# Optimization experiments

Hardware: AMD Instinct MI355X
Metric: run time of the kernel (lower is better)

The kernel has to match this reference:

```python
import jax, jax.numpy as jnp
import numpy as np

B, N, C, M = 2, 16384, 256, 16  # M = win_w*win_h for stage 1
W = N // M

def setup_inputs() -> dict:
    key = jax.random.key(0)
    ks = jax.random.split(key, 8)
    s = 1.0 / np.sqrt(C)
    return {
        "input": jax.random.normal(ks[0], (B, N, C), jnp.float32),
        "embed_qk": jax.random.normal(ks[1], (B, W, M, M, 3), jnp.float32),
        "Wq": jax.random.normal(ks[2], (C, C), jnp.float32) * s,
        "bq": jax.random.normal(ks[3], (C,), jnp.float32) * 0.01,
        "Wk": jax.random.normal(ks[4], (C, C), jnp.float32) * s,
        "bk": jax.random.normal(ks[5], (C,), jnp.float32) * 0.01,
        "Wp": jax.random.normal(ks[6], (3, 1), jnp.float32) * 0.5,
        "bp": jax.random.normal(ks[7], (1,), jnp.float32) * 0.01,
    }

def reference(input, embed_qk, Wq, bq, Wk, bk, Wp, bp):
    WIN = 16  # stage==1 -> win_w*win_h = 4*4
    b, n, c = input.shape
    add = (-n) % WIN
    q = jax.nn.elu(input @ Wq + bq) + 1.0
    k = jax.nn.elu(input @ Wk + bk) + 1.0
    v = input
    pad = ((0, 0), (0, add), (0, 0))
    q_win = jnp.pad(q, pad).reshape(b, -1, WIN, c)
    k_win = jnp.pad(k, pad).reshape(b, -1, WIN, c)
    v_win = jnp.pad(v, pad).reshape(b, -1, WIN, c)
    # second ELU+1 feature map (as in the original)
    phi_q = jax.nn.elu(q_win) + 1.0
    phi_k = jax.nn.elu(k_win) + 1.0
    # KV sums over ALL windows w -> (b, m, c, d)
    KV = jnp.einsum('bwmc,bwmd->bmcd', phi_k, v_win)
    # (b, w, n, m, d) expanded intermediate
    att = jnp.einsum('bwnc,bmcd->bwnmd', phi_q, KV)
    p = (embed_qk @ Wp + bp)[..., 0]  # (b, w, m, m)
    att = att + p[..., None]
    out = att.reshape(b, -1, c)[:, :n, :]
    return out
```

## Files before the change

### kernel.cpp

```cpp
#include <hip/hip_runtime.h>

typedef __attribute__((ext_vector_type(8))) short s16x8;
typedef __attribute__((ext_vector_type(8))) ushort u16x8;
typedef __attribute__((ext_vector_type(4))) ushort u16x4;
typedef __attribute__((ext_vector_type(4))) float f32x4v;

namespace {

constexpr int kB = 2;
constexpr int kN = 16384;
constexpr int kC = 256;
constexpr int kQR = 1024;

__device__ __forceinline__ ushort f2bf(float f) {
  union { float f; uint u; } v; v.f = f;
  uint u = v.u + 0x7fffu + ((v.u >> 16) & 1u);
  return (ushort)(u >> 16);
}

__device__ __forceinline__ float phi_act(float x) {
  return x > 0.f ? x + 2.f : __expf(x) + 1.f;
}

__global__ __launch_bounds__(256) void wt_kernel(const float* __restrict__ Wq,
                                                 const float* __restrict__ Wk,
                                                 ushort* __restrict__ WqT,
                                                 ushort* __restrict__ WkT) {
  __shared__ float ts[64][65];
  const float* W = blockIdx.z ? Wk : Wq;
  ushort* WT = blockIdx.z ? WkT : WqT;
  const int bi = blockIdx.x, bj = blockIdx.y, t = threadIdx.x;
  for (int rep = 0; rep < 16; ++rep) {
    int e = rep * 256 + t, r = e >> 6, c = e & 63;
    ts[r][c] = W[(size_t)(bi * 64 + r) * kC + bj * 64 + c];
  }
  __syncthreads();
  for (int rep = 0; rep < 16; ++rep) {
    int e = rep * 256 + t, j = e >> 6, k = e & 63;
    WT[(size_t)(bj * 64 + j) * kC + bi * 64 + k] = f2bf(ts[k][j]);
  }
}

__global__ __launch_bounds__(256) void regroup_kernel(const float* __restrict__ X,
                                                      ushort* __restrict__ G) {
  __shared__ ushort ls[16 * 288];
  const int cb = blockIdx.x;
  const int wb = blockIdx.y;
  const int b = blockIdx.z;
  const int t = threadIdx.x;
  const float* src = X + ((size_t)b * kN + wb * 256) * kC + cb * 16;
  const int lr = t >> 2, cg = t & 3;
#pragma unroll
  for (int rep = 0; rep < 4; ++rep) {
    int row = rep * 64 + lr;
    float4 v = *reinterpret_cast<const float4*>(src + (size_t)row * kC + cg * 4);
    int w = row >> 4, m = row & 15;
    int base = w * 288 + m * 18 + cg * 4;
    uint p0 = (uint)f2bf(v.x) | ((uint)f2bf(v.y) << 16);
    uint p1 = (uint)f2bf(v.z) | ((uint)f2bf(v.w) << 16);
    *reinterpret_cast<uint*>(ls + base) = p0;
    *reinterpret_cast<uint*>(ls + base + 2) = p1;
  }
  __syncthreads();
  const int m = t >> 4, c_l = t & 15;
#pragma unroll
  for (int oct = 0; oct < 2; ++oct) {
    u16x8 v;
#pragma unroll
    for (int wl = 0; wl < 8; ++wl) v[wl] = ls[(oct * 8 + wl) * 288 + m * 18 + c_l];
    *reinterpret_cast<u16x8*>(
        G + (((size_t)(b * 16 + m) * 128 + wb * 2 + oct) * 256 + cb * 16 + c_l) * 8) = v;
  }
}

__global__ __launch_bounds__(256) void proj_kernel(
    const float* __restrict__ X, const ushort* __restrict__ WqT,
    const ushort* __restrict__ WkT, const float* __restrict__ bq,
    const float* __restrict__ bk, ushort* __restrict__ kg,
    ushort* __restrict__ qf) {
  __shared__ __align__(16) ushort smem[36864];

  const int t = threadIdx.x, lane = t & 63, wv = t >> 6;
  const int bx = blockIdx.x;
  const bool kmode = bx < 1024;
  int b, n0, jb;
  const ushort* WT;
  const float* bias;
  if (kmode) {
    b = bx >> 9; int rem = bx & 511; n0 = (rem >> 1) * 64; jb = bx & 1;
    WT = WkT; bias = bk;
  } else {
    int i = bx - 1024; b = i >> 5; int rem = i & 31; n0 = (rem >> 1) * 64; jb = i & 1;
    WT = WqT; bias = bq;
  }
  const int j0 = jb * 128;
  const float* Xb = X + ((size_t)b * kN + n0) * kC;

  for (int rep = 0; rep < 16; ++rep) {
    int idx = rep * 256 + t;
    int jj = idx >> 5, cc = idx & 31;
    u16x8 v = *reinterpret_cast<const u16x8*>(WT + (size_t)(j0 + jj) * kC + cc * 8);
    *reinterpret_cast<u16x8*>(smem + jj * 256 + ((cc ^ (jj & 31)) << 3)) = v;
  }

  const int aq = t & 7, ar = t >> 3;
  float4 fa0, fa1;
  auto aLoad = [&](int s) {
    fa0 = *reinterpret_cast<const float4*>(Xb + (size_t)ar * kC + s * 32 + aq * 4);
    fa1 = *reinterpret_cast<const float4*>(Xb + (size_t)(ar + 32) * kC + s * 32 + aq * 4);
  };
  auto aWrite = [&](int h) {
    ushort* A = smem + 32768 + h * 2048;
    u16x4 v0 = {f2bf(fa0.x), f2bf(fa0.y), f2bf(fa0.z), f2bf(fa0.w)};
    u16x4 v1 = {f2bf(fa1.x), f2bf(fa1.y), f2bf(fa1.z), f2bf(fa1.w)};
    *reinterpret_cast<u16x4*>(A + ar * 32 + (((aq >> 1) ^ ((ar >> 1) & 3)) << 3) +
                              (aq & 1) * 4) = v0;
    const int r1 = ar + 32;
    *reinterpret_cast<u16x4*>(A + r1 * 32 + (((aq >> 1) ^ ((r1 >> 1) & 3)) << 3) +
                              (aq & 1) * 4) = v1;
  };

  const int lo = lane & 15, hi = lane >> 4;
  const int wr0 = (wv >> 1) * 32, wc0 = (wv & 1) * 64;
  f32x4v acc[2][4] = {};
  auto mma = [&](int h, int s) {
    const ushort* A = smem + 32768 + h * 2048;
    s16x8 a[2], bf[4];
#pragma unroll
    for (int i = 0; i < 2; ++i) {
      int r = wr0 + i * 16 + lo;
      a[i] = *reinterpret_cast<const s16x8*>(A + r * 32 + ((hi ^ ((r >> 1) & 3)) << 3));
    }
#pragma unroll
    for (int fj = 0; fj < 4; ++fj) {
      int j = wc0 + fj * 16 + lo;
      bf[fj] = *reinterpret_cast<const s16x8*>(
          smem + j * 256 + (((s * 4 + hi) ^ (j & 31)) << 3));
    }
#pragma unroll
    for (int i = 0; i < 2; ++i)
#pragma unroll
      for (int fj = 0; fj < 4; ++fj)
        acc[i][fj] = __builtin_amdgcn_mfma_f32_16x16x32_bf16(a[i], bf[fj], acc[i][fj], 0, 0, 0);
  };

  aLoad(0);
  aWrite(0);
  __syncthreads();
  int cur = 0;
  for (int s = 0; s < 8; ++s) {
    if (s < 7) aLoad(s + 1);
    __builtin_amdgcn_sched_barrier(0);
    mma(cur, s);
    __builtin_amdgcn_sched_barrier(0);
    if (s < 7) aWrite(cur ^ 1);
    __syncthreads();
    cur ^= 1;
  }

  float bv[4];
#pragma unroll
  for (int fj = 0; fj < 4; ++fj) bv[fj] = bias[j0 + wc0 + fj * 16 + lo];

  if (kmode) {
    __syncthreads();
    ushort* ep = smem;
#pragma unroll
    for (int i = 0; i < 2; ++i)
#pragma unroll
      for (int fj = 0; fj < 4; ++fj)
#pragma unroll
        for (int r = 0; r < 4; ++r) {
          int row = wr0 + i * 16 + hi * 4 + r;
          int col = wc0 + fj * 16 + lo;
          ep[row * 128 + col] = f2bf(phi_act(acc[i][fj][r] + bv[fj]));
        }
    __syncthreads();
    const int m = t >> 4, cl = t & 15;
    const int wgrp = n0 >> 7, sub = (n0 >> 6) & 1;
#pragma unroll
    for (int rep = 0; rep < 8; ++rep) {
      int c = rep * 16 + cl;
      u16x4 v;
#pragma unroll
      for (int wl = 0; wl < 4; ++wl) v[wl] = ep[(wl * 16 + m) * 128 + c];
      *reinterpret_cast<u16x4*>(
          kg + (((size_t)(b * 16 + m) * 128 + wgrp) * 256 + j0 + c) * 8 + sub * 4) = v;
    }
  } else {
#pragma unroll
    for (int i = 0; i < 2; ++i)
#pragma unroll
      for (int fj = 0; fj < 4; ++fj)
#pragma unroll
        for (int r = 0; r < 4; ++r) {
          int row = n0 + wr0 + i * 16 + hi * 4 + r;
          int col = j0 + wc0 + fj * 16 + lo;
          qf[((size_t)b * kQR + row) * kC + col] = f2bf(phi_act(acc[i][fj][r] + bv[fj]));
        }
  }
}

__global__ __launch_bounds__(256) void kv_kernel(const ushort* __restrict__ kg,
                                                 const ushort* __restrict__ xg,
                                                 ushort* __restrict__ kvt) {
  __shared__ __align__(16) ushort smem[32768];
  const int t = threadIdx.x, lane = t & 63, wv = t >> 6;
  const int swz = (blockIdx.x & 7) * 64 + (blockIdx.x >> 3);
  const int bm = swz >> 4, cb = swz & 3, db = (swz >> 2) & 3;
  const int lc = t & 63, g = t >> 6;
  const ushort* Ab = kg + (size_t)bm * 262144 + (size_t)(cb * 64 + lc) * 8;
  const ushort* Bb = xg + (size_t)bm * 262144 + (size_t)(db * 64 + lc) * 8;

  u16x8 ra[4], rb[4];
  auto sLoad = [&](int s) {
#pragma unroll
    for (int q = 0; q < 4; ++q) {
      const size_t w8 = (size_t)(s * 16 + g + q * 4) * 2048;
      ra[q] = *reinterpret_cast<const u16x8*>(Ab + w8);
      rb[q] = *reinterpret_cast<const u16x8*>(Bb + w8);
    }
  };
  auto sWrite = [&](int h) {
    ushort* A = smem + h * 8192;
    ushort* B = smem + 16384 + h * 8192;
    const int fl = (lc & 15) ^ (lc >> 4);
#pragma unroll
    for (int q = 0; q < 4; ++q) {
      int o = g + q * 4;
      *reinterpret_cast<u16x8*>(A + lc * 128 + ((o ^ fl) << 3)) = ra[q];
      *reinterpret_cast<u16x8*>(B + lc * 128 + ((o ^ fl) << 3)) = rb[q];
    }
  };

  const int lo = lane & 15, hi = lane >> 4;
  const int wr0 = (wv >> 1) * 32, wc0 = (wv & 1) * 32;
  f32x4v acc[2][2] = {};
  auto mma = [&](int h) {
    const ushort* A = smem + h * 8192;
    const ushort* B = smem + 16384 + h * 8192;
#pragma unroll
    for (int kk = 0; kk < 4; ++kk) {
      s16x8 a0, a1, b0, b1;
      {
        int r = wr0 + lo;
        a0 = *reinterpret_cast<const s16x8*>(
            A + r * 128 + (((kk * 4 + hi) ^ ((r & 15) ^ (r >> 4))) << 3));
        int r2 = wr0 + 16 + lo;
        a1 = *reinterpret_cast<const s16x8*>(
            A + r2 * 128 + (((kk * 4 + hi) ^ ((r2 & 15) ^ (r2 >> 4))) << 3));
        int c = wc0 + lo;
        b0 = *reinterpret_cast<const s16x8*>(
            B + c * 128 + (((kk * 4 + hi) ^ ((c & 15) ^ (c >> 4))) << 3));
        int c2 = wc0 + 16 + lo;
        b1 = *reinterpret_cast<const s16x8*>(
            B + c2 * 128 + (((kk * 4 + hi) ^ ((c2 & 15) ^ (c2 >> 4))) << 3));
      }
      acc[0][0] = __builtin_amdgcn_mfma_f32_16x16x32_bf16(a0, b0, acc[0][0], 0, 0, 0);
      acc[0][1] = __builtin_amdgcn_mfma_f32_16x16x32_bf16(a0, b1, acc[0][1], 0, 0, 0);
      acc[1][0] = __builtin_amdgcn_mfma_f32_16x16x32_bf16(a1, b0, acc[1][0], 0, 0, 0);
      acc[1][1] = __builtin_amdgcn_mfma_f32_16x16x32_bf16(a1, b1, acc[1][1], 0, 0, 0);
    }
  };

  sLoad(0);
  sWrite(0);
  __syncthreads();
  int cur = 0;
  for (int s = 0; s < 8; ++s) {
    if (s < 7) sLoad(s + 1);
    __builtin_amdgcn_sched_barrier(0);
    mma(cur);
    __builtin_amdgcn_sched_barrier(0);
    if (s < 7) sWrite(cur ^ 1);
    __syncthreads();
    cur ^= 1;
  }
#pragma unroll
  for (int fi = 0; fi < 2; ++fi)
#pragma unroll
    for (int fj = 0; fj < 2; ++fj) {
      int d = db * 64 + wc0 + fj * 16 + lo;
      int c = cb * 64 + wr0 + fi * 16 + hi * 4;
      u16x4 v = {f2bf(acc[fi][fj][0]), f2bf(acc[fi][fj][1]),
                 f2bf(acc[fi][fj][2]), f2bf(acc[fi][fj][3])};
      *reinterpret_cast<u16x4*>(kvt + ((size_t)bm * 256 + d) * 256 + c) = v;
    }
}

__global__ __launch_bounds__(256) void out_kernel(
    const ushort* __restrict__ qf, const ushort* __restrict__ kvt,
    const float* __restrict__ EQK, const float* __restrict__ Wp,
    const float* __restrict__ bp, float* __restrict__ Out) {
  __shared__ __align__(16) ushort smem[16384];
  __shared__ float Ps[128];
  const int t = threadIdx.x, lane = t & 63, wv = t >> 6;
  const int swz = (blockIdx.x & 7) * 64 + (blockIdx.x >> 3);
  const int bm = swz >> 4, qb = swz & 7, db = (swz >> 3) & 1;
  const int b = bm >> 4, mm = bm & 15;
  if (t < 128) {
    int qr = qb * 128 + t;
    const float* e = EQK + (((size_t)(b * 1024 + (qr >> 4)) * 16 + (qr & 15)) * 16 + mm) * 3;
    Ps[t] = e[0] * Wp[0] + e[1] * Wp[1] + e[2] * Wp[2] + bp[0];
  }
  const int r2 = t >> 2, ch = t & 3;

  u16x8 ra0, ra1, rb0, rb1;
  auto stageLoad = [&](int ks) {
    int k0 = ks * 32;
    const ushort* Aq = qf + ((size_t)b * kQR + qb * 128) * kC;
    const ushort* Bk = kvt + ((size_t)bm * 256 + db * 128) * kC;
    ra0 = *reinterpret_cast<const u16x8*>(Aq + (size_t)r2 * kC + k0 + ch * 8);
    ra1 = *reinterpret_cast<const u16x8*>(Aq + (size_t)(r2 + 64) * kC + k0 + ch * 8);
    rb0 = *reinterpret_cast<const u16x8*>(Bk + (size_t)r2 * kC + k0 + ch * 8);
    rb1 = *reinterpret_cast<const u16x8*>(Bk + (size_t)(r2 + 64) * kC + k0 + ch * 8);
  };
  auto stageWrite = [&](int h) {
    ushort* A = smem + h * 4096;
    ushort* B = smem + 8192 + h * 4096;
    *reinterpret_cast<u16x8*>(A + r2 * 32 + ((ch ^ ((r2 >> 1) & 3)) << 3)) = ra0;
    *reinterpret_cast<u16x8*>(A + (r2 + 64) * 32 + ((ch ^ (((r2 + 64) >> 1) & 3)) << 3)) = ra1;
    *reinterpret_cast<u16x8*>(B + r2 * 32 + ((ch ^ ((r2 >> 1) & 3)) << 3)) = rb0;
    *reinterpret_cast<u16x8*>(B + (r2 + 64) * 32 + ((ch ^ (((r2 + 64) >> 1) & 3)) << 3)) = rb1;
  };

  f32x4v acc[4][4] = {};
  const int lo = lane & 15, hi = lane >> 4;
  const int wr0 = (wv >> 1) * 64, wc0 = (wv & 1) * 64;
  auto mma = [&](int h) {
    const ushort* A = smem + h * 4096;
    const ushort* B = smem + 8192 + h * 4096;
    s16x8 af[4], bf[4];
#pragma unroll
    for (int i = 0; i < 4; ++i) {
      int r = wr0 + i * 16 + lo;
      af[i] = *reinterpret_cast<const s16x8*>(A + r * 32 + ((hi ^ ((r >> 1) & 3)) << 3));
    }
#pragma unroll
    for (int j = 0; j < 4; ++j) {
      int c = wc0 + j * 16 + lo;
      bf[j] = *reinterpret_cast<const s16x8*>(B + c * 32 + ((hi ^ ((c >> 1) & 3)) << 3));
    }
#pragma unroll
    for (int i = 0; i < 4; ++i)
#pragma unroll
      for (int j = 0; j < 4; ++j)
        acc[i][j] = __builtin_amdgcn_mfma_f32_16x16x32_bf16(af[i], bf[j], acc[i][j], 0, 0, 0);
  };

  stageLoad(0);
  stageWrite(0);
  __syncthreads();
  int cur = 0;
  for (int ks = 0; ks < 8; ++ks) {
    if (ks < 7) stageLoad(ks + 1);
    __builtin_amdgcn_sched_barrier(0);
    mma(cur);
    __builtin_amdgcn_sched_barrier(0);
    if (ks < 7) stageWrite(cur ^ 1);
    __syncthreads();
    cur ^= 1;
  }
#pragma unroll
  for (int fi = 0; fi < 4; ++fi)
#pragma unroll
    for (int r4 = 0; r4 < 4; ++r4) {
      int rowl = wr0 + fi * 16 + hi * 4 + r4;
      int qr = qb * 128 + rowl;
      float p = Ps[rowl];
      size_t orow = ((size_t)b * kN + (size_t)qr * 16 + mm) * kC;
#pragma unroll
      for (int fj = 0; fj < 4; ++fj) {
        int d = db * 128 + wc0 + fj * 16 + lo;
        Out[orow + d] = acc[fi][fj][r4] + p;
      }
    }
}

}

extern "C" void kernel_launch(void* const* d_in, const int* in_sizes, int n_in,
                              void* d_out, int out_size, void* d_ws,
                              size_t ws_size, hipStream_t stream) {
  const float* input = (const float*)d_in[0];
  const float* eqk = (const float*)d_in[1];
  const float* Wq = (const float*)d_in[2];
  const float* bq = (const float*)d_in[3];
  const float* Wk = (const float*)d_in[4];
  const float* bk = (const float*)d_in[5];
  const float* Wp = (const float*)d_in[6];
  const float* bp = (const float*)d_in[7];
  float* out = (float*)d_out;

  ushort* ws = (ushort*)d_ws;
  ushort* WqT = ws;
  ushort* WkT = WqT + 65536;
  ushort* xg = WkT + 65536;
  ushort* kg = xg + 8388608;
  ushort* qf = kg + 8388608;
  ushort* kvt = qf + 524288;

  wt_kernel<<<dim3(4, 4, 2), 256, 0, stream>>>(Wq, Wk, WqT, WkT);
  regroup_kernel<<<dim3(16, 64, 2), 256, 0, stream>>>(input, xg);
  proj_kernel<<<dim3(1088), 256, 0, stream>>>(input, WqT, WkT, bq, bk, kg, qf);
  kv_kernel<<<dim3(512), 256, 0, stream>>>(kg, xg, kvt);
  out_kernel<<<dim3(512), 256, 0, stream>>>(qf, kvt, eqk, Wp, bp, out);
}
```

Before: 154.4 us.

## Use direct global-to-LDS loads in projection, KV, and output kernels

Replaces register-staged global loads followed by LDS writes with global_load_lds builtins in the projection weight staging, the KV reduction kernel, and the output GEMM. The KV kernel's LDS layout becomes k-major with no swizzle and keeps double buffering. The output kernel now loads the full K=256 tiles for A and B into 128 KB of LDS at once, replacing its 8-step pipelined loop, with the XOR swizzle moved to the global source address. This aims to cut VGPR pressure and instruction count for staging, but lower occupancy in out_kernel, lost overlap, and possible LDS bank conflicts in the unswizzled KV layout are risks.

```diff
diff --git a/kernel.cpp b/kernel.cpp
--- a/kernel.cpp
+++ b/kernel.cpp
@@ -20,6 +20,12 @@
 
 __device__ __forceinline__ float phi_act(float x) {
   return x > 0.f ? x + 2.f : __expf(x) + 1.f;
+}
+
+__device__ __forceinline__ void gl16(const ushort* g, ushort* l) {
+  __builtin_amdgcn_global_load_lds(
+      (const __attribute__((address_space(1))) void*)g,
+      (__attribute__((address_space(3))) void*)l, 16, 0, 0);
 }
 
 __global__ __launch_bounds__(256) void wt_kernel(const float* __restrict__ Wq,
@@ -99,8 +105,8 @@
   for (int rep = 0; rep < 16; ++rep) {
     int idx = rep * 256 + t;
     int jj = idx >> 5, cc = idx & 31;
-    u16x8 v = *reinterpret_cast<const u16x8*>(WT + (size_t)(j0 + jj) * kC + cc * 8);
-    *reinterpret_cast<u16x8*>(smem + jj * 256 + ((cc ^ (jj & 31)) << 3)) = v;
+    gl16(WT + (size_t)(j0 + jj) * kC + (size_t)(cc ^ (jj & 31)) * 8,
+         smem + idx * 8);
   }
 
   const int aq = t & 7, ar = t >> 3;
@@ -208,54 +214,36 @@
   const int t = threadIdx.x, lane = t & 63, wv = t >> 6;
   const int swz = (blockIdx.x & 7) * 64 + (blockIdx.x >> 3);
   const int bm = swz >> 4, cb = swz & 3, db = (swz >> 2) & 3;
-  const int lc = t & 63, g = t >> 6;
-  const ushort* Ab = kg + (size_t)bm * 262144 + (size_t)(cb * 64 + lc) * 8;
-  const ushort* Bb = xg + (size_t)bm * 262144 + (size_t)(db * 64 + lc) * 8;
-
-  u16x8 ra[4], rb[4];
-  auto sLoad = [&](int s) {
-#pragma unroll
-    for (int q = 0; q < 4; ++q) {
-      const size_t w8 = (size_t)(s * 16 + g + q * 4) * 2048;
-      ra[q] = *reinterpret_cast<const u16x8*>(Ab + w8);
-      rb[q] = *reinterpret_cast<const u16x8*>(Bb + w8);
-    }
-  };
-  auto sWrite = [&](int h) {
+  const int c_l = t & 63;
+  const ushort* Abase = kg + (size_t)bm * 262144 + (size_t)(cb * 64) * 8;
+  const ushort* Bbase = xg + (size_t)bm * 262144 + (size_t)(db * 64) * 8;
+
+  auto STAGE = [&](int h, int s) {
     ushort* A = smem + h * 8192;
     ushort* B = smem + 16384 + h * 8192;
-    const int fl = (lc & 15) ^ (lc >> 4);
-#pragma unroll
-    for (int q = 0; q < 4; ++q) {
-      int o = g + q * 4;
-      *reinterpret_cast<u16x8*>(A + lc * 128 + ((o ^ fl) << 3)) = ra[q];
-      *reinterpret_cast<u16x8*>(B + lc * 128 + ((o ^ fl) << 3)) = rb[q];
+#pragma unroll
+    for (int i = 0; i < 4; ++i) {
+      int o = i * 4 + wv;
+      size_t goff = ((size_t)(s * 16 + o) * 256 + c_l) * 8;
+      int loff = (i * 256 + t) * 8;
+      gl16(Abase + goff, A + loff);
+      gl16(Bbase + goff, B + loff);
     }
   };
 
   const int lo = lane & 15, hi = lane >> 4;
   const int wr0 = (wv >> 1) * 32, wc0 = (wv & 1) * 32;
   f32x4v acc[2][2] = {};
-  auto mma = [&](int h) {
+  auto MMA = [&](int h) {
     const ushort* A = smem + h * 8192;
     const ushort* B = smem + 16384 + h * 8192;
 #pragma unroll
     for (int kk = 0; kk < 4; ++kk) {
-      s16x8 a0, a1, b0, b1;
-      {
-        int r = wr0 + lo;
-        a0 = *reinterpret_cast<const s16x8*>(
-            A + r * 128 + (((kk * 4 + hi) ^ ((r & 15) ^ (r >> 4))) << 3));
-        int r2 = wr0 + 16 + lo;
-        a1 = *reinterpret_cast<const s16x8*>(
-            A + r2 * 128 + (((kk * 4 + hi) ^ ((r2 & 15) ^ (r2 >> 4))) << 3));
-        int c = wc0 + lo;
-        b0 = *reinterpret_cast<const s16x8*>(
-            B + c * 128 + (((kk * 4 + hi) ^ ((c & 15) ^ (c >> 4))) << 3));
-        int c2 = wc0 + 16 + lo;
-        b1 = *reinterpret_cast<const s16x8*>(
-            B + c2 * 128 + (((kk * 4 + hi) ^ ((c2 & 15) ^ (c2 >> 4))) << 3));
-      }
+      const int o = kk * 4 + hi;
+      s16x8 a0 = *reinterpret_cast<const s16x8*>(A + o * 512 + (wr0 + lo) * 8);
+      s16x8 a1 = *reinterpret_cast<const s16x8*>(A + o * 512 + (wr0 + 16 + lo) * 8);
+      s16x8 b0 = *reinterpret_cast<const s16x8*>(B + o * 512 + (wc0 + lo) * 8);
+      s16x8 b1 = *reinterpret_cast<const s16x8*>(B + o * 512 + (wc0 + 16 + lo) * 8);
       acc[0][0] = __builtin_amdgcn_mfma_f32_16x16x32_bf16(a0, b0, acc[0][0], 0, 0, 0);
       acc[0][1] = __builtin_amdgcn_mfma_f32_16x16x32_bf16(a0, b1, acc[0][1], 0, 0, 0);
       acc[1][0] = __builtin_amdgcn_mfma_f32_16x16x32_bf16(a1, b0, acc[1][0], 0, 0, 0);
@@ -263,16 +251,13 @@
     }
   };
 
-  sLoad(0);
-  sWrite(0);
+  STAGE(0, 0);
   __syncthreads();
   int cur = 0;
   for (int s = 0; s < 8; ++s) {
-    if (s < 7) sLoad(s + 1);
+    if (s < 7) STAGE(cur ^ 1, s + 1);
     __builtin_amdgcn_sched_barrier(0);
-    mma(cur);
-    __builtin_amdgcn_sched_barrier(0);
-    if (s < 7) sWrite(cur ^ 1);
+    MMA(cur);
     __syncthreads();
     cur ^= 1;
   }
@@ -292,7 +277,7 @@
     const ushort* __restrict__ qf, const ushort* __restrict__ kvt,
     const float* __restrict__ EQK, const float* __restrict__ Wp,
     const float* __restrict__ bp, float* __restrict__ Out) {
-  __shared__ __align__(16) ushort smem[16384];
+  __shared__ __align__(16) ushort smem[65536];
   __shared__ float Ps[128];
   const int t = threadIdx.x, lane = t & 63, wv = t >> 6;
   const int swz = (blockIdx.x & 7) * 64 + (blockIdx.x >> 3);
@@ -303,63 +288,43 @@
     const float* e = EQK + (((size_t)(b * 1024 + (qr >> 4)) * 16 + (qr & 15)) * 16 + mm) * 3;
     Ps[t] = e[0] * Wp[0] + e[1] * Wp[1] + e[2] * Wp[2] + bp[0];
   }
-  const int r2 = t >> 2, ch = t & 3;
-
-  u16x8 ra0, ra1, rb0, rb1;
-  auto stageLoad = [&](int ks) {
-    int k0 = ks * 32;
-    const ushort* Aq = qf + ((size_t)b * kQR + qb * 128) * kC;
-    const ushort* Bk = kvt + ((size_t)bm * 256 + db * 128) * kC;
-    ra0 = *reinterpret_cast<const u16x8*>(Aq + (size_t)r2 * kC + k0 + ch * 8);
-    ra1 = *reinterpret_cast<const u16x8*>(Aq + (size_t)(r2 + 64) * kC + k0 + ch * 8);
-    rb0 = *reinterpret_cast<const u16x8*>(Bk + (size_t)r2 * kC + k0 + ch * 8);
-    rb1 = *reinterpret_cast<const u16x8*>(Bk + (size_t)(r2 + 64) * kC + k0 + ch * 8);
-  };
-  auto stageWrite = [&](int h) {
-    ushort* A = smem + h * 4096;
-    ushort* B = smem + 8192 + h * 4096;
-    *reinterpret_cast<u16x8*>(A + r2 * 32 + ((ch ^ ((r2 >> 1) & 3)) << 3)) = ra0;
-    *reinterpret_cast<u16x8*>(A + (r2 + 64) * 32 + ((ch ^ (((r2 + 64) >> 1) & 3)) << 3)) = ra1;
-    *reinterpret_cast<u16x8*>(B + r2 * 32 + ((ch ^ ((r2 >> 1) & 3)) << 3)) = rb0;
-    *reinterpret_cast<u16x8*>(B + (r2 + 64) * 32 + ((ch ^ (((r2 + 64) >> 1) & 3)) << 3)) = rb1;
-  };
-
-  f32x4v acc[4][4] = {};
+  const ushort* Aq = qf + ((size_t)b * kQR + qb * 128) * kC;
+  const ushort* Bk = kvt + ((size_t)bm * 256 + db * 128) * kC;
+
+#pragma unroll
+  for (int i = 0; i < 16; ++i) {
+    int S = i * 256 + t;
+    int r = S >> 5, o = S & 31;
+    int osrc = (o & 24) | ((o & 7) ^ (r & 7));
+    gl16(Aq + (size_t)r * kC + osrc * 8, smem + S * 8);
+    gl16(Bk + (size_t)r * kC + osrc * 8, smem + 32768 + S * 8);
+  }
+  __syncthreads();
+
   const int lo = lane & 15, hi = lane >> 4;
   const int wr0 = (wv >> 1) * 64, wc0 = (wv & 1) * 64;
-  auto mma = [&](int h) {
-    const ushort* A = smem + h * 4096;
-    const ushort* B = smem + 8192 + h * 4096;
-    s16x8 af[4], bf[4];
-#pragma unroll
-    for (int i = 0; i < 4; ++i) {
-      int r = wr0 + i * 16 + lo;
-      af[i] = *reinterpret_cast<const s16x8*>(A + r * 32 + ((hi ^ ((r >> 1) & 3)) << 3));
-    }
-#pragma unroll
-    for (int j = 0; j < 4; ++j) {
-      int c = wc0 + j * 16 + lo;
-      bf[j] = *reinterpret_cast<const s16x8*>(B + c * 32 + ((hi ^ ((c >> 1) & 3)) << 3));
-    }
-#pragma unroll
-    for (int i = 0; i < 4; ++i)
-#pragma unroll
-      for (int j = 0; j < 4; ++j)
-        acc[i][j] = __builtin_amdgcn_mfma_f32_16x16x32_bf16(af[i], bf[j], acc[i][j], 0, 0, 0);
-  };
-
-  stageLoad(0);
-  stageWrite(0);
-  __syncthreads();
-  int cur = 0;
-  for (int ks = 0; ks < 8; ++ks) {
-    if (ks < 7) stageLoad(ks + 1);
-    __builtin_amdgcn_sched_barrier(0);
-    mma(cur);
-    __builtin_amdgcn_sched_barrier(0);
-    if (ks < 7) stageWrite(cur ^ 1);
-    __syncthreads();
-    cur ^= 1;
+  f32x4v acc[4][4] = {};
+#pragma unroll
+  for (int kk = 0; kk < 8; ++kk) {
+    const int j = kk * 4 + hi;
+    s16x8 a[4], bf[4];
+#pragma unroll
+    for (int fi = 0; fi < 4; ++fi) {
+      int r = wr0 + fi * 16 + lo;
+      int o = (j & 24) | ((j & 7) ^ (r & 7));
+      a[fi] = *reinterpret_cast<const s16x8*>(smem + r * 256 + o * 8);
+    }
+#pragma unroll
+    for (int fj = 0; fj < 4; ++fj) {
+      int r = wc0 + fj * 16 + lo;
+      int o = (j & 24) | ((j & 7) ^ (r & 7));
+      bf[fj] = *reinterpret_cast<const s16x8*>(smem + 32768 + r * 256 + o * 8);
+    }
+#pragma unroll
+    for (int fi = 0; fi < 4; ++fi)
+#pragma unroll
+      for (int fj = 0; fj < 4; ++fj)
+        acc[fi][fj] = __builtin_amdgcn_mfma_f32_16x16x32_bf16(a[fi], bf[fj], acc[fi][fj], 0, 0, 0);
   }
 #pragma unroll
   for (int fi = 0; fi < 4; ++fi)
```

Measured after the change: 154.0 us. About the same (-0.3%).
